# Performance work log

Hardware: AMD Instinct MI355X
Metric: run time of the kernel (lower is better)

Reference implementation:

```python
import jax, jax.numpy as jnp
import numpy as np

K = 3        # kernel size
PAD = 1      # padding
DG = 16      # deformable groups
MAXR = 10.0  # max_residue_magnitude


def _lrelu(x):
    return jnp.where(x >= 0, x, 0.1 * x)


def _conv3(x, w, b):
    y = jax.lax.conv_general_dilated(x, w, (1, 1), 'SAME',
                                     dimension_numbers=('NCHW', 'OIHW', 'NCHW'))
    return y + b[None, :, None, None]


def _deform_conv2d(x, offset, mask, weight, bias):
    # x: [B,Cin,H,W]; offset: [B,2*DG*K*K,H,W]; mask: [B,DG*K*K,H,W]
    B, Cin, H, W = x.shape
    Cout = weight.shape[0]
    G, Cg, K2 = DG, Cin // DG, K * K
    off = offset.reshape(B, G, K2, 2, H, W)
    dy, dx = off[:, :, :, 0], off[:, :, :, 1]
    ky = jnp.repeat(jnp.arange(K), K).astype(x.dtype)   # [K2]
    kx = jnp.tile(jnp.arange(K), K).astype(x.dtype)
    hh = jnp.arange(H, dtype=x.dtype)
    ww = jnp.arange(W, dtype=x.dtype)
    # sampling positions [B,G,K2,H,W]
    py = dy + ky[None, None, :, None, None] + hh[None, None, None, :, None] - PAD
    px = dx + kx[None, None, :, None, None] + ww[None, None, None, None, :] - PAD
    y0 = jnp.floor(py)
    x0 = jnp.floor(px)
    wy1 = py - y0
    wx1 = px - x0
    xf = x.reshape(B, G, Cg, H * W)

    def gather(yi, xi, wgt):
        valid = (yi >= 0) & (yi <= H - 1) & (xi >= 0) & (xi <= W - 1)
        idx = (jnp.clip(yi, 0, H - 1).astype(jnp.int32) * W
               + jnp.clip(xi, 0, W - 1).astype(jnp.int32)).reshape(B, G, -1)
        vals = jnp.take_along_axis(
            xf, jnp.broadcast_to(idx[:, :, None, :], (B, G, Cg, idx.shape[-1])), axis=3)
        vals = vals.reshape(B, G, Cg, K2, H, W)
        w = (wgt * valid.astype(x.dtype))[:, :, None]  # [B,G,1,K2,H,W]
        return vals * w

    s = (gather(y0, x0, (1 - wy1) * (1 - wx1))
         + gather(y0, x0 + 1, (1 - wy1) * wx1)
         + gather(y0 + 1, x0, wy1 * (1 - wx1))
         + gather(y0 + 1, x0 + 1, wy1 * wx1))
    s = s * mask.reshape(B, G, K2, H, W)[:, :, None]
    wr = weight.reshape(Cout, G, Cg, K2)
    out = jnp.einsum('ogck,bgckhw->bohw', wr, s)
    return out + bias[None, :, None, None]


def setup_inputs() -> dict:
    key = jax.random.key(0)
    ks = jax.random.split(key, 16)
    B, Cin, Cout, H, W = 4, 128, 64, 96, 96
    Coff = 3 * Cout + 4  # 196
    stdv = 1.0 / np.sqrt(Cin * K * K)
    inp = {
        'x': jax.random.normal(ks[0], (B, Cin, H, W), jnp.float32),
        'extra_feat': jax.random.normal(ks[1], (B, 3 * Cout, H, W), jnp.float32),
        'flow_1': jax.random.normal(ks[2], (B, 2, H, W), jnp.float32),
        'flow_2': jax.random.normal(ks[3], (B, 2, H, W), jnp.float32),
        'weight': jax.random.uniform(ks[4], (Cout, Cin, K, K), jnp.float32, -stdv, stdv),
        'bias': jax.random.normal(ks[5], (Cout,), jnp.float32) * 0.01,
        'ow0': jax.random.normal(ks[6], (Cout, Coff, K, K), jnp.float32) * 0.02,
        'ob0': jnp.zeros((Cout,), jnp.float32),
        'ow1': jax.random.normal(ks[7], (Cout, Cout, K, K), jnp.float32) * 0.02,
        'ob1': jnp.zeros((Cout,), jnp.float32),
        'ow2': jax.random.normal(ks[8], (Cout, Cout, K, K), jnp.float32) * 0.02,
        'ob2': jnp.zeros((Cout,), jnp.float32),
        'ow3': jax.random.normal(ks[9], (27 * DG, Cout, K, K), jnp.float32) * 0.01,
        'ob3': jnp.zeros((27 * DG,), jnp.float32),
    }
    return inp


def reference(x, extra_feat, flow_1, flow_2, weight, bias,
              ow0, ob0, ow1, ob1, ow2, ob2, ow3, ob3):
    feat = jnp.concatenate([extra_feat, flow_1, flow_2], axis=1)
    h = _lrelu(_conv3(feat, ow0, ob0))
    h = _lrelu(_conv3(h, ow1, ob1))
    h = _lrelu(_conv3(h, ow2, ob2))
    out = _conv3(h, ow3, ob3)
    o1, o2, m = jnp.split(out, 3, axis=1)
    offs = MAXR * jnp.tanh(jnp.concatenate([o1, o2], axis=1))
    off1, off2 = jnp.split(offs, 2, axis=1)
    off1 = off1 + jnp.tile(flow_1[:, ::-1], (1, off1.shape[1] // 2, 1, 1))
    off2 = off2 + jnp.tile(flow_2[:, ::-1], (1, off2.shape[1] // 2, 1, 1))
    offset = jnp.concatenate([off1, off2], axis=1)
    mask = jax.nn.sigmoid(m)
    return _deform_conv2d(x, offset, mask, weight, bias)
```

## Files before the change

kernel.cpp:

```cpp
#include <hip/hip_runtime.h>
#include <math.h>

#define HW 9216
#define Hh 96
#define Ww 96
#define PHW 9604
#define QSLOTS 9604

typedef __attribute__((ext_vector_type(8))) short bh8;
typedef __attribute__((ext_vector_type(4))) short bh4;
typedef __attribute__((ext_vector_type(4))) float f32x4;
typedef __attribute__((ext_vector_type(2))) float f32x2;
typedef __attribute__((ext_vector_type(4))) int i32x4;
union bh8i { bh8 v; i32x4 i; };

__device__ __forceinline__ short f2bf(float f) {
    union { float f; unsigned u; } v; v.f = f;
    unsigned r = v.u + 0x7FFFu + ((v.u >> 16) & 1u);
    return (short)(r >> 16);
}
__device__ __forceinline__ float bf2f(short s) {
    union { unsigned u; float f; } v; v.u = ((unsigned)(unsigned short)s) << 16;
    return v.f;
}
__device__ __forceinline__ float lo_bf(unsigned u) {
    union { unsigned u; float f; } v; v.u = u << 16; return v.f;
}
__device__ __forceinline__ float hi_bf(unsigned u) {
    union { unsigned u; float f; } v; v.u = u & 0xFFFF0000u; return v.f;
}
__device__ __forceinline__ int cvt_pk_bf16(float lo, float hi) {
    int r;
    asm("v_cvt_pk_bf16_f32 %0, %1, %2" : "=v"(r) : "v"(lo), "v"(hi));
    return r;
}

__global__ void prep_misc(short* __restrict__ xpad1, short* __restrict__ hpa,
                          short* __restrict__ hpb, short* __restrict__ xdp,
                          const float* __restrict__ ow0, const float* __restrict__ ow1,
                          const float* __restrict__ ow2, const float* __restrict__ ow3,
                          const float* __restrict__ wd,
                          short* __restrict__ wb0, short* __restrict__ wb1,
                          short* __restrict__ wb2, short* __restrict__ wb3,
                          short* __restrict__ wbd) {
    int i = blockIdx.x * 256 + threadIdx.x;
    const int z1 = 4 * 388 * 224, z2 = 4 * 388 * 64;
    if (i < z1 + 2 * z2) {
        short* p; int C;
        if (i < z1) { p = xpad1; C = 224; }
        else if (i < z1 + z2) { p = hpa; C = 64; i -= z1; }
        else { p = hpb; C = 64; i -= z1 + z2; }
        int c = i % C;
        int r = i / C;
        int b = r / 388, pid = r - b * 388;
        int row, col;
        if (pid < 98)       { row = 0;  col = pid; }
        else if (pid < 196) { row = 97; col = pid - 98; }
        else if (pid < 292) { row = pid - 196 + 1; col = 0; }
        else                { row = pid - 292 + 1; col = 97; }
        p[((size_t)b * PHW + row * 98 + col) * C + c] = 0;
        return;
    }
    i -= z1 + 2 * z2;
    const int zr = 64 * 579 * 4;
    if (i < zr) {
        int piece = i & 3;
        int r2 = i >> 2;
        int s = r2 % 579, bg = r2 / 579;
        int y, x;
        if (s < 98)       { y = 0;  x = s; }
        else if (s < 196) { y = 96; x = s - 98; }
        else if (s < 294) { y = 97; x = s - 196; }
        else {
            int s2 = s - 294;
            int xi = s2 / 95;
            x = (xi == 0) ? 0 : ((xi == 1) ? 96 : 97);
            y = 1 + s2 - xi * 95;
        }
        *(bh8*)&xdp[(((size_t)bg * QSLOTS) + y * 98 + x) * 32 + piece * 8] =
            (bh8){0, 0, 0, 0, 0, 0, 0, 0};
        return;
    }
    i -= zr;
    const int n0 = 64 * 9 * 224, n1 = 64 * 9 * 64, n3 = 448 * 9 * 64, nd = 144 * 64 * 8;
    if (i < n0) {
        int co = i / (9 * 224); int r = i - co * (9 * 224);
        int tap = r / 224, ci = r - tap * 224;
        wb0[i] = f2bf(ci < 196 ? ow0[(co * 196 + ci) * 9 + tap] : 0.f);
        return;
    }
    i -= n0;
    if (i < n1) {
        int co = i / (9 * 64); int r = i - co * (9 * 64);
        int tap = r / 64, ci = r - tap * 64;
        wb1[i] = f2bf(ow1[(co * 64 + ci) * 9 + tap]);
        return;
    }
    i -= n1;
    if (i < n1) {
        int co = i / (9 * 64); int r = i - co * (9 * 64);
        int tap = r / 64, ci = r - tap * 64;
        wb2[i] = f2bf(ow2[(co * 64 + ci) * 9 + tap]);
        return;
    }
    i -= n1;
    if (i < n3) {
        int co = i / (9 * 64); int r = i - co * (9 * 64);
        int tap = r / 64, ci = r - tap * 64;
        wb3[i] = f2bf(co < 432 ? ow3[(co * 64 + ci) * 9 + tap] : 0.f);
        return;
    }
    i -= n3;
    if (i < nd) {
        int gt = i >> 9, r = i & 511;
        int co = r >> 3, c = r & 7;
        int g = gt / 9, tap = gt - g * 9;
        wbd[i] = f2bf(wd[(co * 128 + g * 8 + c) * 9 + tap]);
    }
}

__global__ void pack_all(const float* __restrict__ extra,
                         const float* __restrict__ f1,
                         const float* __restrict__ f2,
                         const float* __restrict__ x,
                         short* __restrict__ xp,
                         short* __restrict__ xdp) {
    __shared__ float t[32][33];
    const int tid = threadIdx.x, tx = tid & 31, ty = tid >> 5;
    const int pt = blockIdx.x, b = blockIdx.z;
    if (blockIdx.y < 7) {
        const int ct = blockIdx.y;
#pragma unroll
        for (int j = 0; j < 4; ++j) {
            int ch = ct * 32 + ty + j * 8;
            int p = pt * 32 + tx;
            float v = 0.f;
            if (ch < 192)      v = extra[(b * 192 + ch) * HW + p];
            else if (ch < 194) v = f1[(b * 2 + ch - 192) * HW + p];
            else if (ch < 196) v = f2[(b * 2 + ch - 194) * HW + p];
            t[ty + j * 8][tx] = v;
        }
        __syncthreads();
#pragma unroll
        for (int j = 0; j < 4; ++j) {
            int pr = ty + j * 8;
            int p = pt * 32 + pr;
            int r = p / 96, c = p - r * 96;
            xp[((size_t)b * PHW + (r + 1) * 98 + (c + 1)) * 224 + ct * 32 + tx] =
                f2bf(t[tx][pr]);
        }
    } else {
        const int ct = blockIdx.y - 7;
#pragma unroll
        for (int j = 0; j < 4; ++j) {
            int ch = ct * 32 + ty + j * 8;
            t[ty + j * 8][tx] = x[((size_t)b * 128 + ch) * HW + pt * 32 + tx];
        }
        __syncthreads();
        if (tid < 128) {
            int oct = tid >> 5, p = tid & 31;
            int g = ct * 4 + oct;
            int pix = pt * 32 + p;
            int r = pix / 96, c = pix - r * 96;
            bh8 v;
#pragma unroll
            for (int cc = 0; cc < 8; ++cc) v[cc] = f2bf(t[oct * 8 + cc][p]);
            size_t sb = ((size_t)b * 16 + g) * QSLOTS;
            int pr = r + 1, pc = c + 1;
            *(bh8*)&xdp[(sb + pr * 98 + pc) * 32 + 0]        = v;
            *(bh8*)&xdp[(sb + pr * 98 + pc - 1) * 32 + 8]    = v;
            *(bh8*)&xdp[(sb + (pr - 1) * 98 + pc) * 32 + 16] = v;
            *(bh8*)&xdp[(sb + (pr - 1) * 98 + pc - 1) * 32 + 24] = v;
        }
    }
}

template<int CINP, int KCH>
__launch_bounds__(256)
__global__ void conv_mfma(const short* __restrict__ xp,
                          const short* __restrict__ wb,
                          const float* __restrict__ bias,
                          short* __restrict__ o1) {
    __shared__ __attribute__((aligned(16))) short smA[9 * 64 * 32];
    const int tid = threadIdx.x;
    const int lane = tid & 63, wv = tid >> 6;
    const int q = lane >> 4, l15 = lane & 15;
    const int b = blockIdx.y;
    const int pix0 = blockIdx.x * 64 + wv * 16;
    const int soh = pix0 / 96, sow = pix0 - (pix0 / 96) * 96;

    const short* bp = xp + ((size_t)b * PHW + soh * 98 + sow + l15) * CINP + q * 8;

    const int sco = tid >> 2, sqq = tid & 3;
    const short* wsrc = wb + (size_t)sco * (9 * CINP) + sqq * 8;

    f32x4 acc[4];
#pragma unroll
    for (int t = 0; t < 4; ++t) acc[t] = (f32x4){0.f, 0.f, 0.f, 0.f};

    for (int p = 0; p < KCH; ++p) {
        __syncthreads();
        bh8 wtmp[9];
#pragma unroll
        for (int tap = 0; tap < 9; ++tap)
            wtmp[tap] = *(const bh8*)(wsrc + tap * CINP + p * 32);
#pragma unroll
        for (int tap = 0; tap < 9; ++tap)
            *(bh8*)&smA[tap * 2048 + sco * 32 + sqq * 8] = wtmp[tap];
        __syncthreads();
#pragma unroll
        for (int tap = 0; tap < 9; ++tap) {
            const int ky = tap / 3, kx = tap - (tap / 3) * 3;
            bh8 bf = *(const bh8*)(bp + (ky * 98 + kx) * CINP + p * 32);
#pragma unroll
            for (int t = 0; t < 4; ++t) {
                bh8 af = *(const bh8*)&smA[tap * 2048 + (t * 16 + l15) * 32 + q * 8];
                acc[t] = __builtin_amdgcn_mfma_f32_16x16x32_bf16(af, bf, acc[t], 0, 0, 0);
            }
        }
    }

    size_t base = ((size_t)b * PHW + (soh + 1) * 98 + sow + l15 + 1) * 64;
#pragma unroll
    for (int t = 0; t < 4; ++t) {
        bh4 v4;
#pragma unroll
        for (int r = 0; r < 4; ++r) {
            int co = t * 16 + q * 4 + r;
            float v = acc[t][r] + bias[co];
            v = (v >= 0.f) ? v : 0.1f * v;
            v4[r] = f2bf(v);
        }
        *(bh4*)(o1 + base + t * 16 + q * 4) = v4;
    }
}

__launch_bounds__(256)
__global__ void conv4_mfma(const short* __restrict__ xp,
                           const short* __restrict__ wb,
                           const float* __restrict__ bias,
                           float* __restrict__ offp,
                           short* __restrict__ maskb,
                           const float* __restrict__ flow1,
                           const float* __restrict__ flow2) {
    __shared__ __attribute__((aligned(16))) short smA[9 * 64 * 32];
    const int tid = threadIdx.x;
    const int lane = tid & 63, wv = tid >> 6;
    const int q = lane >> 4, l15 = lane & 15;
    const int b = blockIdx.y;
    const int cob = blockIdx.z * 64;
    const int pix0 = blockIdx.x * 64 + wv * 16;
    const int soh = pix0 / 96, sow = pix0 - (pix0 / 96) * 96;

    const short* bp = xp + ((size_t)b * PHW + soh * 98 + sow + l15) * 64 + q * 8;

    const int sco = tid >> 2, sqq = tid & 3;
    const short* wsrc = wb + (size_t)(cob + sco) * 576 + sqq * 8;

    f32x4 acc[4];
#pragma unroll
    for (int t = 0; t < 4; ++t) acc[t] = (f32x4){0.f, 0.f, 0.f, 0.f};

    for (int p = 0; p < 2; ++p) {
        __syncthreads();
        bh8 wtmp[9];
#pragma unroll
        for (int tap = 0; tap < 9; ++tap)
            wtmp[tap] = *(const bh8*)(wsrc + tap * 64 + p * 32);
#pragma unroll
        for (int tap = 0; tap < 9; ++tap)
            *(bh8*)&smA[tap * 2048 + sco * 32 + sqq * 8] = wtmp[tap];
        __syncthreads();
#pragma unroll
        for (int tap = 0; tap < 9; ++tap) {
            const int ky = tap / 3, kx = tap - (tap / 3) * 3;
            bh8 bf = *(const bh8*)(bp + (ky * 98 + kx) * 64 + p * 32);
#pragma unroll
            for (int t = 0; t < 4; ++t) {
                bh8 af = *(const bh8*)&smA[tap * 2048 + (t * 16 + l15) * 32 + q * 8];
                acc[t] = __builtin_amdgcn_mfma_f32_16x16x32_bf16(af, bf, acc[t], 0, 0, 0);
            }
        }
    }

    const int pix = pix0 + l15;
#pragma unroll
    for (int t = 0; t < 4; ++t) {
        int cb0 = cob + t * 16 + q * 4;
        if (cb0 < 288) {
            const float* fl = (cb0 < 144) ? flow1 : flow2;
            float fe = fl[(b * 2 + 1) * HW + pix];
            float fo = fl[(b * 2) * HW + pix];
            float t0 = 10.f * tanhf(acc[t][0] + bias[cb0 + 0]) + fe;
            float t1 = 10.f * tanhf(acc[t][1] + bias[cb0 + 1]) + fo;
            float t2 = 10.f * tanhf(acc[t][2] + bias[cb0 + 2]) + fe;
            float t3 = 10.f * tanhf(acc[t][3] + bias[cb0 + 3]) + fo;
            size_t p0 = ((size_t)b * 144 + (cb0 >> 1)) * HW + pix;
            *(f32x2*)&offp[p0 * 2] = (f32x2){t0, t1};
            *(f32x2*)&offp[(p0 + HW) * 2] = (f32x2){t2, t3};
        } else {
#pragma unroll
            for (int r = 0; r < 4; ++r) {
                int chn = cb0 + r;
                if (chn < 432) {
                    float v = acc[t][r] + bias[chn];
                    maskb[((size_t)b * 144 + (chn - 288)) * HW + pix] =
                        f2bf(1.f / (1.f + expf(-v)));
                }
            }
        }
    }
}

__launch_bounds__(256)
__global__ void deform_mfma(const short* __restrict__ xdp,
                            const float* __restrict__ offp,
                            const short* __restrict__ maskb,
                            const short* __restrict__ wbd,
                            const float* __restrict__ bias,
                            float* __restrict__ out) {
    __shared__ float red[4][1024];
    const int tid = threadIdx.x;
    const int lane = tid & 63, wv = tid >> 6;
    const int q = lane >> 4, l15 = lane & 15;
    const int blk = blockIdx.x;
    const int xs = blk & 7, idx = blk >> 3;
    const int b = xs >> 1;
    const int pix0 = ((xs & 1) * 288 + idx) * 16;
    const int pix = pix0 + l15;
    const int h = pix / 96, w = pix - (pix / 96) * 96;

    const short* xb = xdp + (size_t)b * 16 * QSLOTS * 32;

    f32x4 acc[4];
#pragma unroll
    for (int t = 0; t < 4; ++t) acc[t] = (f32x4){0.f, 0.f, 0.f, 0.f};

#pragma unroll
    for (int chunk = 0; chunk < 4; ++chunk) {
        const int g = wv * 4 + chunk;
        const float* opp = offp + (((size_t)b * 144 + g * 9) * HW + pix) * 2;
        const short* mp  = maskb + ((size_t)b * 144 + g * 9) * HW + pix;

        f32x2 dxy[9];
        float mk[9];
#pragma unroll
        for (int i = 0; i < 9; ++i) {
            dxy[i] = *(const f32x2*)(opp + (size_t)i * HW * 2);
            mk[i]  = bf2f(mp[(size_t)i * HW]);
        }

        int soff[9];
        float wq[9];
#pragma unroll
        for (int i = 0; i < 9; ++i) {
            float py = dxy[i][0] + (float)(i / 3) + (float)h - 1.f;
            float px = dxy[i][1] + (float)(i % 3) + (float)w - 1.f;
            py = fminf(fmaxf(py, -1.f), 96.f);
            px = fminf(fmaxf(px, -1.f), 96.f);
            float y0f = floorf(py), x0f = floorf(px);
            float wy1 = py - y0f, wx1 = px - x0f;
            int yp = (int)y0f + 1, xp = (int)x0f + 1;
            soff[i] = ((g * QSLOTS + yp * 98 + xp) << 5) + q * 8;
            float wy = (q & 2) ? wy1 : (1.f - wy1);
            float wx = (q & 1) ? wx1 : (1.f - wx1);
            wq[i] = wy * wx * mk[i];
        }

#pragma unroll
        for (int i = 0; i < 9; ++i) {
            bh8i cv;
            cv.v = *(const bh8*)(xb + soff[i]);
            const f32x2 w2 = (f32x2){wq[i], wq[i]};
            bh8i bf;
#pragma unroll
            for (int k2 = 0; k2 < 4; ++k2) {
                unsigned u = (unsigned)cv.i[k2];
                f32x2 pv = (f32x2){lo_bf(u), hi_bf(u)} * w2;
                bf.i[k2] = cvt_pk_bf16(pv[0], pv[1]);
            }
            const int gt = g * 9 + i;
            const short* ap = wbd + ((size_t)gt * 64 + l15) * 8;
#pragma unroll
            for (int t = 0; t < 4; ++t) {
                bh8 af = *(const bh8*)(ap + t * 128);
                acc[t] = __builtin_amdgcn_mfma_f32_16x16x32_bf16(af, bf.v, acc[t], 0, 0, 0);
            }
        }
    }

#pragma unroll
    for (int t = 0; t < 4; ++t)
#pragma unroll
        for (int r = 0; r < 4; ++r)
            red[wv][(t * 16 + q * 4 + r) * 16 + l15] = acc[t][r];
    __syncthreads();
    for (int e = tid; e < 1024; e += 256) {
        int co = e >> 4, pl = e & 15;
        float v = red[0][e] + red[1][e] + red[2][e] + red[3][e] + bias[co];
        out[((size_t)b * 64 + co) * HW + pix0 + pl] = v;
    }
}

extern "C" void kernel_launch(void* const* d_in, const int* in_sizes, int n_in,
                              void* d_out, int out_size, void* d_ws, size_t ws_size,
                              hipStream_t stream) {
    const float* x      = (const float*)d_in[0];
    const float* extra  = (const float*)d_in[1];
    const float* flow1  = (const float*)d_in[2];
    const float* flow2  = (const float*)d_in[3];
    const float* weight = (const float*)d_in[4];
    const float* bias   = (const float*)d_in[5];
    const float* ow0    = (const float*)d_in[6];
    const float* ob0    = (const float*)d_in[7];
    const float* ow1    = (const float*)d_in[8];
    const float* ob1    = (const float*)d_in[9];
    const float* ow2    = (const float*)d_in[10];
    const float* ob2    = (const float*)d_in[11];
    const float* ow3    = (const float*)d_in[12];
    const float* ob3    = (const float*)d_in[13];
    float* out = (float*)d_out;

    char* wsb = (char*)d_ws;
    short* xpad1 = (short*)wsb;   wsb += (size_t)4 * PHW * 224 * 2;
    short* hpa   = (short*)wsb;   wsb += (size_t)4 * PHW * 64 * 2;
    short* hpb   = (short*)wsb;   wsb += (size_t)4 * PHW * 64 * 2;
    float* offpair = (float*)wsb; wsb += (size_t)4 * 144 * HW * 2 * 4;
    short* maskbuf = (short*)wsb; wsb += (size_t)4 * 144 * HW * 2;
    short* xdp     = (short*)wsb; wsb += (size_t)4 * 16 * QSLOTS * 32 * 2 + 64;
    short* wb0     = (short*)wsb; wsb += 64 * 9 * 224 * 2;
    short* wb1     = (short*)wsb; wsb += 64 * 9 * 64 * 2;
    short* wb2     = (short*)wsb; wsb += 64 * 9 * 64 * 2;
    short* wb3     = (short*)wsb; wsb += 448 * 9 * 64 * 2;
    short* wbd     = (short*)wsb;

    const int prep_total = 546304 + 148224 + 534528;
    prep_misc<<<dim3((prep_total + 255) / 256), 256, 0, stream>>>(
        xpad1, hpa, hpb, xdp, ow0, ow1, ow2, ow3, weight,
        wb0, wb1, wb2, wb3, wbd);
    pack_all<<<dim3(288, 11, 4), 256, 0, stream>>>(extra, flow1, flow2, x, xpad1, xdp);

    conv_mfma<224, 7><<<dim3(144, 4), 256, 0, stream>>>(xpad1, wb0, ob0, hpa);
    conv_mfma<64, 2><<<dim3(144, 4), 256, 0, stream>>>(hpa, wb1, ob1, hpb);
    conv_mfma<64, 2><<<dim3(144, 4), 256, 0, stream>>>(hpb, wb2, ob2, hpa);
    conv4_mfma<<<dim3(144, 4, 7), 256, 0, stream>>>(hpa, wb3, ob3, offpair,
                                                    maskbuf, flow1, flow2);
    deform_mfma<<<dim3(2304), 256, 0, stream>>>(xdp, offpair, maskbuf, wbd, bias, out);
}
```

Baseline: 325.7 us.

## Store deform input once per pixel and gather four bilinear corners per lane

The deformable-conv input buffer used to hold four shifted copies of each pixel's 8-channel group, so a lane could fetch one bilinear corner with a single load. It now holds one padded copy, and each lane loads all four corners itself and blends them in fp32 before building the MFMA operand. The K dimension is remapped so each quarter-wave covers a different (group, tap) pair, with the deform weights rearranged to match. This cuts the xdp buffer and its pack-time writes to a quarter, and halves the offset and mask loads per lane, at the cost of four gathers per tap per lane instead of one.

```diff
diff --git a/kernel.cpp b/kernel.cpp
--- a/kernel.cpp
+++ b/kernel.cpp
@@ -5,7 +5,6 @@
 #define Hh 96
 #define Ww 96
 #define PHW 9604
-#define QSLOTS 9604
 
 typedef __attribute__((ext_vector_type(8))) short bh8;
 typedef __attribute__((ext_vector_type(4))) short bh4;
@@ -62,27 +61,22 @@
         return;
     }
     i -= z1 + 2 * z2;
-    const int zr = 64 * 579 * 4;
+    const int zr = 4 * 16 * 388 * 8;
     if (i < zr) {
-        int piece = i & 3;
-        int r2 = i >> 2;
-        int s = r2 % 579, bg = r2 / 579;
-        int y, x;
-        if (s < 98)       { y = 0;  x = s; }
-        else if (s < 196) { y = 96; x = s - 98; }
-        else if (s < 294) { y = 97; x = s - 196; }
-        else {
-            int s2 = s - 294;
-            int xi = s2 / 95;
-            x = (xi == 0) ? 0 : ((xi == 1) ? 96 : 97);
-            y = 1 + s2 - xi * 95;
-        }
-        *(bh8*)&xdp[(((size_t)bg * QSLOTS) + y * 98 + x) * 32 + piece * 8] =
-            (bh8){0, 0, 0, 0, 0, 0, 0, 0};
+        int c8 = i & 7;
+        int r = i >> 3;
+        int pid = r % 388;
+        int bg = r / 388;
+        int row, col;
+        if (pid < 98)       { row = 0;  col = pid; }
+        else if (pid < 196) { row = 97; col = pid - 98; }
+        else if (pid < 292) { row = pid - 196 + 1; col = 0; }
+        else                { row = pid - 292 + 1; col = 97; }
+        xdp[((size_t)bg * PHW + row * 98 + col) * 8 + c8] = 0;
         return;
     }
     i -= zr;
-    const int n0 = 64 * 9 * 224, n1 = 64 * 9 * 64, n3 = 448 * 9 * 64, nd = 144 * 64 * 8;
+    const int n0 = 64 * 9 * 224, n1 = 64 * 9 * 64, n3 = 448 * 9 * 64, nd = 64 * 1152;
     if (i < n0) {
         int co = i / (9 * 224); int r = i - co * (9 * 224);
         int tap = r / 224, ci = r - tap * 224;
@@ -112,8 +106,8 @@
     }
     i -= n3;
     if (i < nd) {
-        int gt = i >> 9, r = i & 511;
-        int co = r >> 3, c = r & 7;
+        int co = i / 1152, kd = i - co * 1152;
+        int gt = kd >> 3, c = kd & 7;
         int g = gt / 9, tap = gt - g * 9;
         wbd[i] = f2bf(wd[(co * 128 + g * 8 + c) * 9 + tap]);
     }
@@ -165,12 +159,7 @@
             bh8 v;
 #pragma unroll
             for (int cc = 0; cc < 8; ++cc) v[cc] = f2bf(t[oct * 8 + cc][p]);
-            size_t sb = ((size_t)b * 16 + g) * QSLOTS;
-            int pr = r + 1, pc = c + 1;
-            *(bh8*)&xdp[(sb + pr * 98 + pc) * 32 + 0]        = v;
-            *(bh8*)&xdp[(sb + pr * 98 + pc - 1) * 32 + 8]    = v;
-            *(bh8*)&xdp[(sb + (pr - 1) * 98 + pc) * 32 + 16] = v;
-            *(bh8*)&xdp[(sb + (pr - 1) * 98 + pc - 1) * 32 + 24] = v;
+            *(bh8*)&xdp[(((size_t)b * 16 + g) * PHW + (r + 1) * 98 + (c + 1)) * 8] = v;
         }
     }
 }
@@ -330,62 +319,70 @@
     const int pix = pix0 + l15;
     const int h = pix / 96, w = pix - (pix / 96) * 96;
 
-    const short* xb = xdp + (size_t)b * 16 * QSLOTS * 32;
+    const float* opp = offp + ((size_t)b * 144 * HW + pix) * 2;
+    const short* mp = maskb + (size_t)b * 144 * HW + pix;
+    const short* xb = xdp + (size_t)b * 16 * PHW * 8;
+    const short* ap = wbd + (size_t)l15 * 1152 + wv * 288 + q * 8;
+
+    f32x2 dxy[9];
+    float mk[9];
+#pragma unroll
+    for (int i = 0; i < 9; ++i) {
+        const int gt = wv * 36 + i * 4 + q;
+        dxy[i] = *(const f32x2*)(opp + (size_t)gt * HW * 2);
+        mk[i] = bf2f(mp[(size_t)gt * HW]);
+    }
+
+    const short* cp[9];
+    f32x4 ww[9];
+#pragma unroll
+    for (int i = 0; i < 9; ++i) {
+        const int gt = wv * 36 + i * 4 + q;
+        const int g = gt / 9, tap = gt - (gt / 9) * 9;
+        float py = dxy[i][0] + (float)(tap / 3) + (float)h - 1.f;
+        float px = dxy[i][1] + (float)(tap - (tap / 3) * 3) + (float)w - 1.f;
+        py = fminf(fmaxf(py, -1.f), 96.f);
+        px = fminf(fmaxf(px, -1.f), 96.f);
+        float y0f = floorf(py), x0f = floorf(px);
+        float wy1 = py - y0f, wx1 = px - x0f;
+        float wy0 = 1.f - wy1, wx0 = 1.f - wx1;
+        int yp = (int)y0f + 1, xp = (int)x0f + 1;
+        cp[i] = xb + ((size_t)g * PHW + yp * 98 + xp) * 8;
+        float m = mk[i];
+        ww[i] = (f32x4){wy0 * wx0 * m, wy0 * wx1 * m, wy1 * wx0 * m, wy1 * wx1 * m};
+    }
 
     f32x4 acc[4];
 #pragma unroll
     for (int t = 0; t < 4; ++t) acc[t] = (f32x4){0.f, 0.f, 0.f, 0.f};
 
 #pragma unroll
-    for (int chunk = 0; chunk < 4; ++chunk) {
-        const int g = wv * 4 + chunk;
-        const float* opp = offp + (((size_t)b * 144 + g * 9) * HW + pix) * 2;
-        const short* mp  = maskb + ((size_t)b * 144 + g * 9) * HW + pix;
-
-        f32x2 dxy[9];
-        float mk[9];
-#pragma unroll
-        for (int i = 0; i < 9; ++i) {
-            dxy[i] = *(const f32x2*)(opp + (size_t)i * HW * 2);
-            mk[i]  = bf2f(mp[(size_t)i * HW]);
-        }
-
-        int soff[9];
-        float wq[9];
-#pragma unroll
-        for (int i = 0; i < 9; ++i) {
-            float py = dxy[i][0] + (float)(i / 3) + (float)h - 1.f;
-            float px = dxy[i][1] + (float)(i % 3) + (float)w - 1.f;
-            py = fminf(fmaxf(py, -1.f), 96.f);
-            px = fminf(fmaxf(px, -1.f), 96.f);
-            float y0f = floorf(py), x0f = floorf(px);
-            float wy1 = py - y0f, wx1 = px - x0f;
-            int yp = (int)y0f + 1, xp = (int)x0f + 1;
-            soff[i] = ((g * QSLOTS + yp * 98 + xp) << 5) + q * 8;
-            float wy = (q & 2) ? wy1 : (1.f - wy1);
-            float wx = (q & 1) ? wx1 : (1.f - wx1);
-            wq[i] = wy * wx * mk[i];
-        }
-
-#pragma unroll
-        for (int i = 0; i < 9; ++i) {
-            bh8i cv;
-            cv.v = *(const bh8*)(xb + soff[i]);
-            const f32x2 w2 = (f32x2){wq[i], wq[i]};
-            bh8i bf;
-#pragma unroll
-            for (int k2 = 0; k2 < 4; ++k2) {
-                unsigned u = (unsigned)cv.i[k2];
-                f32x2 pv = (f32x2){lo_bf(u), hi_bf(u)} * w2;
-                bf.i[k2] = cvt_pk_bf16(pv[0], pv[1]);
-            }
-            const int gt = g * 9 + i;
-            const short* ap = wbd + ((size_t)gt * 64 + l15) * 8;
-#pragma unroll
-            for (int t = 0; t < 4; ++t) {
-                bh8 af = *(const bh8*)(ap + t * 128);
-                acc[t] = __builtin_amdgcn_mfma_f32_16x16x32_bf16(af, bf.v, acc[t], 0, 0, 0);
-            }
+    for (int i = 0; i < 9; ++i) {
+        bh8i c00, c01, c10, c11;
+        c00.v = *(const bh8*)(cp[i]);
+        c01.v = *(const bh8*)(cp[i] + 8);
+        c10.v = *(const bh8*)(cp[i] + 98 * 8);
+        c11.v = *(const bh8*)(cp[i] + 99 * 8);
+        const f32x2 W00 = (f32x2){ww[i][0], ww[i][0]};
+        const f32x2 W01 = (f32x2){ww[i][1], ww[i][1]};
+        const f32x2 W10 = (f32x2){ww[i][2], ww[i][2]};
+        const f32x2 W11 = (f32x2){ww[i][3], ww[i][3]};
+        bh8i bf;
+#pragma unroll
+        for (int k = 0; k < 4; ++k) {
+            unsigned u00 = (unsigned)c00.i[k], u01 = (unsigned)c01.i[k];
+            unsigned u10 = (unsigned)c10.i[k], u11 = (unsigned)c11.i[k];
+            f32x2 p00 = (f32x2){lo_bf(u00), hi_bf(u00)};
+            f32x2 p01 = (f32x2){lo_bf(u01), hi_bf(u01)};
+            f32x2 p10 = (f32x2){lo_bf(u10), hi_bf(u10)};
+            f32x2 p11 = (f32x2){lo_bf(u11), hi_bf(u11)};
+            f32x2 s = p00 * W00 + p01 * W01 + p10 * W10 + p11 * W11;
+            bf.i[k] = cvt_pk_bf16(s[0], s[1]);
+        }
+#pragma unroll
+        for (int t = 0; t < 4; ++t) {
+            bh8 af = *(const bh8*)(ap + (size_t)t * 16 * 1152 + i * 32);
+            acc[t] = __builtin_amdgcn_mfma_f32_16x16x32_bf16(af, bf.v, acc[t], 0, 0, 0);
         }
     }
 
@@ -427,14 +424,14 @@
     short* hpb   = (short*)wsb;   wsb += (size_t)4 * PHW * 64 * 2;
     float* offpair = (float*)wsb; wsb += (size_t)4 * 144 * HW * 2 * 4;
     short* maskbuf = (short*)wsb; wsb += (size_t)4 * 144 * HW * 2;
-    short* xdp     = (short*)wsb; wsb += (size_t)4 * 16 * QSLOTS * 32 * 2 + 64;
+    short* xdp     = (short*)wsb; wsb += (size_t)4 * 16 * PHW * 8 * 2 + 32;
     short* wb0     = (short*)wsb; wsb += 64 * 9 * 224 * 2;
     short* wb1     = (short*)wsb; wsb += 64 * 9 * 64 * 2;
     short* wb2     = (short*)wsb; wsb += 64 * 9 * 64 * 2;
     short* wb3     = (short*)wsb; wsb += 448 * 9 * 64 * 2;
     short* wbd     = (short*)wsb;
 
-    const int prep_total = 546304 + 148224 + 534528;
+    const int prep_total = 546304 + 198656 + 534528;
     prep_misc<<<dim3((prep_total + 255) / 256), 256, 0, stream>>>(
         xpad1, hpa, hpb, xdp, ow0, ow1, ow2, ow3, weight,
         wb0, wb1, wb2, wb3, wbd);
```

Result: faster. 299.5 us (-8.0%).
